# Kernel optimization log

Measured on AMD Instinct MI355X. Metric: run time of the kernel, lower is better.

## Reference

```python
import jax, jax.numpy as jnp
import numpy as np

Q_H, KV_H, DIM = 32, 8, 4096
HEAD_DIM = DIM // Q_H
FACTOR = Q_H // KV_H
BS, SL = 2, 2048


def setup_inputs() -> dict:
    key = jax.random.key(0)
    ks = jax.random.split(key, 9)
    s_in = 1.0 / np.sqrt(DIM)
    x = jax.random.normal(ks[0], (BS, SL, DIM), dtype=jnp.float32)
    wq_w = jax.random.uniform(ks[1], (DIM, Q_H * HEAD_DIM), jnp.float32, -s_in, s_in)
    wq_b = jax.random.uniform(ks[2], (Q_H * HEAD_DIM,), jnp.float32, -s_in, s_in)
    wk_w = jax.random.uniform(ks[3], (DIM, KV_H * HEAD_DIM), jnp.float32, -s_in, s_in)
    wk_b = jax.random.uniform(ks[4], (KV_H * HEAD_DIM,), jnp.float32, -s_in, s_in)
    wv_w = jax.random.uniform(ks[5], (DIM, KV_H * HEAD_DIM), jnp.float32, -s_in, s_in)
    wv_b = jax.random.uniform(ks[6], (KV_H * HEAD_DIM,), jnp.float32, -s_in, s_in)
    wo_w = jax.random.uniform(ks[7], (DIM, DIM), jnp.float32, -s_in, s_in)
    wo_b = jax.random.uniform(ks[8], (DIM,), jnp.float32, -s_in, s_in)
    return {"x": x, "wq_w": wq_w, "wq_b": wq_b, "wk_w": wk_w, "wk_b": wk_b,
            "wv_w": wv_w, "wv_b": wv_b, "wo_w": wo_w, "wo_b": wo_b}


def reference(x, wq_w, wq_b, wk_w, wk_b, wv_w, wv_b, wo_w, wo_b):
    bs, sl, _ = x.shape
    # projections
    q = (x @ wq_w + wq_b).reshape(bs, sl, Q_H, HEAD_DIM)          # [b,s,Hq,d]
    k = (x @ wk_w + wk_b).reshape(bs, sl, KV_H, HEAD_DIM)         # [b,s,Hkv,d]
    v = (x @ wv_w + wv_b).reshape(bs, sl, KV_H, HEAD_DIM)
    # group queries by kv head: [b,s,Hkv,factor,d]
    qg = q.reshape(bs, sl, KV_H, FACTOR, HEAD_DIM)
    scale = 1.0 / jnp.sqrt(jnp.asarray(HEAD_DIM, x.dtype))
    # scores: broadcast kv heads instead of physically repeating
    attn = jnp.einsum('bqhfd,bkhd->bhfqk', qg, k) * scale          # [b,Hkv,f,Sq,Sk]
    att = jax.nn.softmax(attn, axis=-1)
    a = jnp.einsum('bhfqk,bkhd->bqhfd', att, v)                    # [b,Sq,Hkv,f,d]
    a = a.reshape(bs, sl, DIM)
    return a @ wo_w + wo_b
```

## Files before the change

### kernel.cpp

```cpp
#include <hip/hip_runtime.h>
#include <math.h>


typedef unsigned short u16;
typedef unsigned int u32;
typedef __bf16 bf16x8 __attribute__((ext_vector_type(8)));
typedef float f32x4 __attribute__((ext_vector_type(4)));
typedef float f32x16 __attribute__((ext_vector_type(16)));
typedef unsigned short u16x8 __attribute__((ext_vector_type(8)));
typedef unsigned short u16x4 __attribute__((ext_vector_type(4)));

#define MFMA16(a, b, c) __builtin_amdgcn_mfma_f32_16x16x32_bf16((a), (b), (c), 0, 0, 0)
#define MFMA32(a, b, c) __builtin_amdgcn_mfma_f32_32x32x16_bf16((a), (b), (c), 0, 0, 0)

#define GLDS(gp, lp)                                                      \
  __builtin_amdgcn_global_load_lds(                                       \
      (const __attribute__((address_space(1))) unsigned int*)(gp),        \
      (__attribute__((address_space(3))) unsigned int*)(lp), 16, 0, 0)

__device__ __forceinline__ u16 f2b(float f) {
  unsigned b = __float_as_uint(f);
  b += 0x7fffu + ((b >> 16) & 1u);
  return (u16)(b >> 16);
}

__device__ __forceinline__ u32 pk2(float a, float b) {
  union { __bf16 h[2]; u32 w; } u;
  u.h[0] = (__bf16)a;
  u.h[1] = (__bf16)b;
  return u.w;
}

__global__ __launch_bounds__(256) void cast_f32_bf16(const float* __restrict__ in,
                                                     u16* __restrict__ out, int n) {
  int i = (blockIdx.x * 256 + threadIdx.x) * 8;
  if (i >= n) return;
  f32x4 a = *(const f32x4*)&in[i];
  f32x4 b = *(const f32x4*)&in[i + 4];
  u16x8 v;
#pragma unroll
  for (int j = 0; j < 4; j++) { v[j] = f2b(a[j]); v[4 + j] = f2b(b[j]); }
  *(u16x8*)&out[i] = v;
}

__global__ __launch_bounds__(256) void transpose_cast(const float* __restrict__ in,
                                                      u16* __restrict__ out,
                                                      int R, int C) {
  __shared__ u16 t[32][33];
  const int lc = threadIdx.x & 31;
  const int lr = threadIdx.x >> 5;
  const int c0 = blockIdx.x * 32, r0 = blockIdx.y * 32;
#pragma unroll
  for (int i = 0; i < 4; i++) {
    int r = lr + i * 8;
    t[r][lc] = f2b(in[(size_t)(r0 + r) * C + c0 + lc]);
  }
  __syncthreads();
#pragma unroll
  for (int i = 0; i < 4; i++) {
    int r = lr + i * 8;
    out[(size_t)(c0 + r) * R + r0 + lc] = t[lc][r];
  }
}

template <int STORE_T, int OUT_F32>
__global__ __launch_bounds__(256, 2) void gemm_bt(const u16* __restrict__ A,
                                                  const u16* __restrict__ BT,
                                                  const float* __restrict__ bias,
                                                  void* __restrict__ Cv,
                                                  int M, int N) {
  __shared__ u16 As[128][64];
  __shared__ u16 Bs[128][64];
  const int tid = threadIdx.x;
  const int lane = tid & 63, wave = tid >> 6;
  const int l15 = lane & 15, quad = lane >> 4;
  const int m0 = blockIdx.y * 128, n0 = blockIdx.x * 128;
  const int wm = (wave >> 1) * 64, wn = (wave & 1) * 64;
  const int srow = wave * 32 + (lane >> 3);
  const int scol = (lane & 7) * 8;
  const u16* gA = &A[(size_t)(m0 + srow) * 4096 + scol];
  const u16* gB = &BT[(size_t)(n0 + srow) * 4096 + scol];
  f32x4 acc[4][4] = {};
  for (int kb = 0; kb < 4096; kb += 64) {
    __syncthreads();
#pragma unroll
    for (int j = 0; j < 4; j++) {
      GLDS(gA + (size_t)j * 8 * 4096 + kb, &As[wave * 32 + j * 8][0]);
      GLDS(gB + (size_t)j * 8 * 4096 + kb, &Bs[wave * 32 + j * 8][0]);
    }
    __syncthreads();
#pragma unroll
    for (int ks = 0; ks < 2; ks++) {
      bf16x8 a[4], b[4];
#pragma unroll
      for (int mt = 0; mt < 4; mt++)
        a[mt] = *(const bf16x8*)&As[wm + mt * 16 + l15][ks * 32 + quad * 8];
#pragma unroll
      for (int nt = 0; nt < 4; nt++)
        b[nt] = *(const bf16x8*)&Bs[wn + nt * 16 + l15][ks * 32 + quad * 8];
#pragma unroll
      for (int mt = 0; mt < 4; mt++)
#pragma unroll
        for (int nt = 0; nt < 4; nt++)
          acc[mt][nt] = MFMA16(a[mt], b[nt], acc[mt][nt]);
    }
  }
  float bv[4];
#pragma unroll
  for (int nt = 0; nt < 4; nt++) bv[nt] = bias[n0 + wn + nt * 16 + l15];
#pragma unroll
  for (int mt = 0; mt < 4; mt++) {
    const int row = m0 + wm + mt * 16 + quad * 4;
#pragma unroll
    for (int nt = 0; nt < 4; nt++) {
      const int col = n0 + wn + nt * 16 + l15;
      if (STORE_T) {
        u16x4 v;
#pragma unroll
        for (int r = 0; r < 4; r++) v[r] = f2b(acc[mt][nt][r] + bv[nt]);
        *(u16x4*)&((u16*)Cv)[(size_t)col * M + row] = v;
      } else if (OUT_F32) {
#pragma unroll
        for (int r = 0; r < 4; r++)
          ((float*)Cv)[(size_t)(row + r) * N + col] = acc[mt][nt][r] + bv[nt];
      } else {
#pragma unroll
        for (int r = 0; r < 4; r++)
          ((u16*)Cv)[(size_t)(row + r) * N + col] = f2b(acc[mt][nt][r] + bv[nt]);
      }
    }
  }
}

#define STAGE_KV(bf, t)                                                          \
  {                                                                              \
    _Pragma("unroll") for (int i_ = 0; i_ < 4; i_++) {                           \
      GLDS(gK + (size_t)((t) * 64 + i_ * 4) * 1024 + (offK ^ ((i_ & 1) << 5)),   \
           &KsB[bf][(wave * 16 + i_ * 4) * 128]);                                \
      GLDS(gV + (size_t)(i_ * 8) * 4096 + (t) * 64,                              \
           &VsB[bf][(wave * 32 + i_ * 8) * 64]);                                 \
    }                                                                            \
  }

__global__ __launch_bounds__(256, 2) void flash_gqa(const u16* __restrict__ K,
                                                    const u16* __restrict__ VT,
                                                    u16* __restrict__ QO) {
  __shared__ __align__(16) u16 KsB[2][64 * 128];
  __shared__ __align__(16) u16 VsB[2][128 * 64];
  const int tid = threadIdx.x;
  const int lane = tid & 63, wave = tid >> 6;
  const int l31 = lane & 31, hi = lane >> 5;
  const int bx = blockIdx.x;
  const int qt = bx & 15, h = (bx >> 4) & 31, b = bx >> 9;
  const int hk = h >> 2;
  const int qrow0 = b * 2048 + qt * 128 + wave * 32;
  const float scl2 = 0.08838834764831845f * 1.4426950408889634f;

  const int offK = ((lane & 15) * 8) ^ ((lane >> 4) << 3);
  const u16* gK = &K[(size_t)(b * 2048 + wave * 16 + (lane >> 4)) * 1024 + hk * 128];
  const u16* gV = &VT[(size_t)(hk * 128 + wave * 32 + (lane >> 3)) * 4096 + b * 2048 +
                      (((lane & 7) * 8) ^ ((lane >> 3) << 3))];

  STAGE_KV(0, 0);

  bf16x8 qf[8];
#pragma unroll
  for (int ks = 0; ks < 8; ks++)
    qf[ks] = *(const bf16x8*)&QO[(size_t)(qrow0 + l31) * 4096 + h * 128 + ks * 16 + hi * 8];

  f32x16 o[4] = {};
  float mrun = -3.0e38f, lrun = 0.0f;

  __syncthreads();

  for (int t = 0; t < 32; t++) {
    const int bf = t & 1;
    if (t < 31) STAGE_KV(bf ^ 1, t + 1);

    f32x16 st[2] = {};
    __builtin_amdgcn_s_setprio(1);
#pragma unroll
    for (int ks = 0; ks < 8; ks++) {
#pragma unroll
      for (int kvt = 0; kvt < 2; kvt++) {
        const int row = kvt * 32 + l31;
        bf16x8 kf = *(const bf16x8*)&KsB[bf][row * 128 +
                                            ((ks * 16 + hi * 8) ^ ((row & 7) << 3))];
        st[kvt] = MFMA32(kf, qf[ks], st[kvt]);
      }
    }
    __builtin_amdgcn_s_setprio(0);

    float tm[16];
#pragma unroll
    for (int r = 0; r < 16; r++) tm[r] = fmaxf(st[0][r], st[1][r]);
#pragma unroll
    for (int s = 8; s >= 1; s >>= 1)
#pragma unroll
      for (int r = 0; r < s; r++) tm[r] = fmaxf(tm[r], tm[r + s]);
    float mx = fmaxf(tm[0], __shfl_xor(tm[0], 32, 64));
    const float mxs = mx * scl2;
    if (__any(mxs > mrun + 8.0f)) {
      const float mn = fmaxf(mrun, mxs);
      const float alpha = __builtin_amdgcn_exp2f(mrun - mn);
      mrun = mn;
      lrun *= alpha;
#pragma unroll
      for (int re = 0; re < 16; re++) {
        const float av = __shfl(alpha, (re & 3) + 8 * (re >> 2) + 4 * hi, 64);
#pragma unroll
        for (int dt = 0; dt < 4; dt++) o[dt][re] *= av;
      }
    }
    float rsa[4] = {0.f, 0.f, 0.f, 0.f};
#pragma unroll
    for (int kvt = 0; kvt < 2; kvt++)
#pragma unroll
      for (int r = 0; r < 16; r++) {
        const float p = __builtin_amdgcn_exp2f(fmaf(st[kvt][r], scl2, -mrun));
        st[kvt][r] = p;
        rsa[r & 3] += p;
      }
    float rs = (rsa[0] + rsa[1]) + (rsa[2] + rsa[3]);
    rs += __shfl_xor(rs, 32, 64);
    lrun += rs;

    u32 W0[8], W1[8];
#pragma unroll
    for (int rp = 0; rp < 8; rp++) {
      W0[rp] = pk2(st[0][2 * rp], st[0][2 * rp + 1]);
      W1[rp] = pk2(st[1][2 * rp], st[1][2 * rp + 1]);
    }
    u32 fw[4][4];
#pragma unroll
    for (int kvs = 0; kvs < 4; kvs++) {
#pragma unroll
      for (int sl = 0; sl < 2; sl++) {
        const u32 wa = (kvs < 2) ? W0[4 * (kvs & 1) + sl] : W1[4 * (kvs & 1) + sl];
        const u32 wb = (kvs < 2) ? W0[4 * (kvs & 1) + 2 + sl] : W1[4 * (kvs & 1) + 2 + sl];
        const u32 own = hi ? wb : wa;
        const u32 snd = hi ? wa : wb;
        const u32 rcv = (u32)__shfl_xor((int)snd, 32, 64);
        fw[kvs][sl] = hi ? rcv : own;
        fw[kvs][2 + sl] = hi ? own : rcv;
      }
    }

    __builtin_amdgcn_s_setprio(1);
#pragma unroll
    for (int kvs = 0; kvs < 4; kvs++) {
      union { u32 w[4]; bf16x8 v; } pa;
      pa.w[0] = fw[kvs][0]; pa.w[1] = fw[kvs][1];
      pa.w[2] = fw[kvs][2]; pa.w[3] = fw[kvs][3];
#pragma unroll
      for (int dt = 0; dt < 4; dt++) {
        const int row = dt * 32 + l31;
        bf16x8 vf = *(const bf16x8*)&VsB[bf][row * 64 +
                                            ((kvs * 16 + hi * 8) ^ ((row & 7) << 3))];
        o[dt] = MFMA32(pa.v, vf, o[dt]);
      }
    }
    __builtin_amdgcn_s_setprio(0);

    __syncthreads();
  }

  const float invl = 1.0f / lrun;
#pragma unroll
  for (int re = 0; re < 16; re++) {
    const int qv = (re & 3) + 8 * (re >> 2) + 4 * hi;
    const float il = __shfl(invl, qv, 64);
    const size_t rowb = (size_t)(qrow0 + qv) * 4096 + h * 128;
#pragma unroll
    for (int dt = 0; dt < 4; dt++)
      QO[rowb + dt * 32 + l31] = f2b(o[dt][re] * il);
  }
}

extern "C" void kernel_launch(void* const* d_in, const int* in_sizes, int n_in,
                              void* d_out, int out_size, void* d_ws, size_t ws_size,
                              hipStream_t stream) {
  (void)in_sizes; (void)n_in; (void)out_size; (void)ws_size;
  const float* x    = (const float*)d_in[0];
  const float* wq_w = (const float*)d_in[1];
  const float* wq_b = (const float*)d_in[2];
  const float* wk_w = (const float*)d_in[3];
  const float* wk_b = (const float*)d_in[4];
  const float* wv_w = (const float*)d_in[5];
  const float* wv_b = (const float*)d_in[6];
  const float* wo_w = (const float*)d_in[7];
  const float* wo_b = (const float*)d_in[8];
  float* out = (float*)d_out;
  char* ws = (char*)d_ws;
  char* od = (char*)d_out;

  u16* TQ  = (u16*)(ws);
  u16* QA  = (u16*)(ws + 33554432);
  u16* Xb  = (u16*)(od);
  u16* TK  = (u16*)(od + 33554432);
  u16* TV  = (u16*)(od + 41943040);
  u16* Kb  = (u16*)(od + 50331648);
  u16* VTb = (u16*)(od + 58720256);

  cast_f32_bf16<<<8192, 256, 0, stream>>>(x, Xb, 16777216);
  transpose_cast<<<dim3(128, 128), 256, 0, stream>>>(wq_w, TQ, 4096, 4096);
  transpose_cast<<<dim3(32, 128), 256, 0, stream>>>(wk_w, TK, 4096, 1024);
  transpose_cast<<<dim3(32, 128), 256, 0, stream>>>(wv_w, TV, 4096, 1024);

  gemm_bt<0, 0><<<dim3(32, 32), 256, 0, stream>>>(Xb, TQ, wq_b, QA, 4096, 4096);
  gemm_bt<0, 0><<<dim3(8, 32), 256, 0, stream>>>(Xb, TK, wk_b, Kb, 4096, 1024);
  gemm_bt<1, 0><<<dim3(8, 32), 256, 0, stream>>>(Xb, TV, wv_b, VTb, 4096, 1024);

  transpose_cast<<<dim3(128, 128), 256, 0, stream>>>(wo_w, TQ, 4096, 4096);

  flash_gqa<<<dim3(1024), 256, 0, stream>>>(Kb, VTb, QA);

  gemm_bt<0, 1><<<dim3(32, 32), 256, 0, stream>>>(QA, TQ, wo_b, out, 4096, 4096);
}
```

Measured before the change: 886.4 us.

## Single-buffer V tile, raise occupancy to 3 blocks, use permlane32_swap

V is now single-buffered in LDS and loaded within the same iteration, with an extra barrier before the PV MFMAs. Only K stays double-buffered. This cuts LDS per block from 64KB to 48KB, so launch bounds can go to 3 blocks per CU. Cross-half reductions and the P-fragment exchange now use permlane32_swap instead of ds shuffles, and the max reduction is flattened. The trade-off is that V load latency is no longer hidden by the previous iteration and each iteration adds a sync, while register pressure rises under the tighter launch bound.

```diff
diff --git a/kernel.cpp b/kernel.cpp
--- a/kernel.cpp
+++ b/kernel.cpp
@@ -9,6 +9,7 @@
 typedef float f32x16 __attribute__((ext_vector_type(16)));
 typedef unsigned short u16x8 __attribute__((ext_vector_type(8)));
 typedef unsigned short u16x4 __attribute__((ext_vector_type(4)));
+typedef int i32x2 __attribute__((ext_vector_type(2)));
 
 #define MFMA16(a, b, c) __builtin_amdgcn_mfma_f32_16x16x32_bf16((a), (b), (c), 0, 0, 0)
 #define MFMA32(a, b, c) __builtin_amdgcn_mfma_f32_32x32x16_bf16((a), (b), (c), 0, 0, 0)
@@ -132,21 +133,24 @@
   }
 }
 
-#define STAGE_KV(bf, t)                                                          \
-  {                                                                              \
-    _Pragma("unroll") for (int i_ = 0; i_ < 4; i_++) {                           \
-      GLDS(gK + (size_t)((t) * 64 + i_ * 4) * 1024 + (offK ^ ((i_ & 1) << 5)),   \
-           &KsB[bf][(wave * 16 + i_ * 4) * 128]);                                \
-      GLDS(gV + (size_t)(i_ * 8) * 4096 + (t) * 64,                              \
-           &VsB[bf][(wave * 32 + i_ * 8) * 64]);                                 \
-    }                                                                            \
-  }
-
-__global__ __launch_bounds__(256, 2) void flash_gqa(const u16* __restrict__ K,
+#define STAGE_K(bf, t)                                                         \
+  {                                                                            \
+    _Pragma("unroll") for (int i_ = 0; i_ < 4; i_++)                           \
+      GLDS(gK + (size_t)((t) * 64 + i_ * 4) * 1024 + (offK ^ ((i_ & 1) << 5)), \
+           &KsB[bf][(wave * 16 + i_ * 4) * 128]);                              \
+  }
+#define STAGE_V(t)                                                             \
+  {                                                                            \
+    _Pragma("unroll") for (int i_ = 0; i_ < 4; i_++)                           \
+      GLDS(gV + (size_t)(i_ * 8) * 4096 + (t) * 64,                            \
+           &Vs[(wave * 32 + i_ * 8) * 64]);                                    \
+  }
+
+__global__ __launch_bounds__(256, 3) void flash_gqa(const u16* __restrict__ K,
                                                     const u16* __restrict__ VT,
                                                     u16* __restrict__ QO) {
   __shared__ __align__(16) u16 KsB[2][64 * 128];
-  __shared__ __align__(16) u16 VsB[2][128 * 64];
+  __shared__ __align__(16) u16 Vs[128 * 64];
   const int tid = threadIdx.x;
   const int lane = tid & 63, wave = tid >> 6;
   const int l31 = lane & 31, hi = lane >> 5;
@@ -161,7 +165,7 @@
   const u16* gV = &VT[(size_t)(hk * 128 + wave * 32 + (lane >> 3)) * 4096 + b * 2048 +
                       (((lane & 7) * 8) ^ ((lane >> 3) << 3))];
 
-  STAGE_KV(0, 0);
+  STAGE_K(0, 0);
 
   bf16x8 qf[8];
 #pragma unroll
@@ -175,7 +179,8 @@
 
   for (int t = 0; t < 32; t++) {
     const int bf = t & 1;
-    if (t < 31) STAGE_KV(bf ^ 1, t + 1);
+    STAGE_V(t);
+    if (t < 31) STAGE_K(bf ^ 1, t + 1);
 
     f32x16 st[2] = {};
     __builtin_amdgcn_s_setprio(1);
@@ -191,14 +196,17 @@
     }
     __builtin_amdgcn_s_setprio(0);
 
-    float tm[16];
-#pragma unroll
-    for (int r = 0; r < 16; r++) tm[r] = fmaxf(st[0][r], st[1][r]);
-#pragma unroll
-    for (int s = 8; s >= 1; s >>= 1)
-#pragma unroll
-      for (int r = 0; r < s; r++) tm[r] = fmaxf(tm[r], tm[r + s]);
-    float mx = fmaxf(tm[0], __shfl_xor(tm[0], 32, 64));
+    float m8[8];
+#pragma unroll
+    for (int r = 0; r < 8; r++)
+      m8[r] = fmaxf(fmaxf(fmaxf(st[0][r], st[0][r + 8]), st[1][r]), st[1][r + 8]);
+    float mA = fmaxf(fmaxf(m8[0], m8[1]), m8[2]);
+    mA = fmaxf(fmaxf(mA, m8[3]), m8[4]);
+    mA = fmaxf(fmaxf(mA, m8[5]), m8[6]);
+    mA = fmaxf(mA, m8[7]);
+    i32x2 mr = __builtin_amdgcn_permlane32_swap(__float_as_int(mA), __float_as_int(mA),
+                                                false, false);
+    const float mx = fmaxf(__int_as_float(mr[0]), __int_as_float(mr[1]));
     const float mxs = mx * scl2;
     if (__any(mxs > mrun + 8.0f)) {
       const float mn = fmaxf(mrun, mxs);
@@ -222,8 +230,9 @@
         rsa[r & 3] += p;
       }
     float rs = (rsa[0] + rsa[1]) + (rsa[2] + rsa[3]);
-    rs += __shfl_xor(rs, 32, 64);
-    lrun += rs;
+    i32x2 rr = __builtin_amdgcn_permlane32_swap(__float_as_int(rs), __float_as_int(rs),
+                                                false, false);
+    lrun += __int_as_float(rr[0]) + __int_as_float(rr[1]);
 
     u32 W0[8], W1[8];
 #pragma unroll
@@ -238,13 +247,13 @@
       for (int sl = 0; sl < 2; sl++) {
         const u32 wa = (kvs < 2) ? W0[4 * (kvs & 1) + sl] : W1[4 * (kvs & 1) + sl];
         const u32 wb = (kvs < 2) ? W0[4 * (kvs & 1) + 2 + sl] : W1[4 * (kvs & 1) + 2 + sl];
-        const u32 own = hi ? wb : wa;
-        const u32 snd = hi ? wa : wb;
-        const u32 rcv = (u32)__shfl_xor((int)snd, 32, 64);
-        fw[kvs][sl] = hi ? rcv : own;
-        fw[kvs][2 + sl] = hi ? own : rcv;
-      }
-    }
+        i32x2 r = __builtin_amdgcn_permlane32_swap((int)wa, (int)wb, false, false);
+        fw[kvs][sl] = (u32)r[0];
+        fw[kvs][2 + sl] = (u32)r[1];
+      }
+    }
+
+    __syncthreads();
 
     __builtin_amdgcn_s_setprio(1);
 #pragma unroll
@@ -255,8 +264,8 @@
 #pragma unroll
       for (int dt = 0; dt < 4; dt++) {
         const int row = dt * 32 + l31;
-        bf16x8 vf = *(const bf16x8*)&VsB[bf][row * 64 +
-                                            ((kvs * 16 + hi * 8) ^ ((row & 7) << 3))];
+        bf16x8 vf = *(const bf16x8*)&Vs[row * 64 +
+                                        ((kvs * 16 + hi * 8) ^ ((row & 7) << 3))];
         o[dt] = MFMA32(pa.v, vf, o[dt]);
       }
     }
```

Result: no change. 876.5 us (-1.1%).
